# Performance work log

Hardware: AMD Instinct MI355X
Metric: run time of the kernel (lower is better)

The kernel has to match this reference:

```python
import jax, jax.numpy as jnp
import numpy as np

# Dims: B samples, D=2048 backbone feature dim (resnet50 fc.in_features),
B, D, G, R, K, C = 16384, 2048, 8, 6, 3, 16


def setup_inputs() -> dict:
    key = jax.random.key(0)
    k0, k1, k2, k3 = jax.random.split(key, 4)
    feats = jax.random.normal(k0, (B, D), dtype=jnp.float32)          # backbone output (dropout=eval identity)
    roi_ids = jax.random.randint(k1, (B,), 0, G)                       # per-sample routing id (roi_names)
    W_reg = jax.random.normal(k2, (G, R, D), dtype=jnp.float32) * 0.02  # reg_heads[roi].weight
    b_reg = jnp.zeros((G, R), dtype=jnp.float32)                       # reg_heads[roi].bias
    W_cls = jax.random.normal(k3, (G, K, C, D), dtype=jnp.float32) * 0.02  # cls_heads[roi][k].weight
    b_cls = jnp.zeros((G, K, C), dtype=jnp.float32)                    # cls_heads[roi][k].bias
    return {"feats": feats, "roi_ids": roi_ids, "W_reg": W_reg, "b_reg": b_reg,
            "W_cls": W_cls, "b_cls": b_cls}


def reference(feats, roi_ids, W_reg, b_reg, W_cls, b_cls):
    # Original loop applies, per sample i, the Linear heads of roi_names[i].
    # Vectorized: compute all-ROI head outputs densely, then gather the routed one.
    # (Same math per sample; dropout is identity in eval mode.)
    reg_all = jnp.einsum('bd,grd->bgr', feats, W_reg) + b_reg[None]        # [B, G, R]
    cls_all = jnp.einsum('bd,gkcd->bgkc', feats, W_cls) + b_cls[None]      # [B, G, K, C]
    reg = jnp.take_along_axis(reg_all, roi_ids[:, None, None], axis=1)[:, 0]            # [B, R]
    cls = jnp.take_along_axis(cls_all, roi_ids[:, None, None, None], axis=1)[:, 0]      # [B, K, C]
    return reg, cls
```

## Files before the change

kernel.cpp:

```cpp
#include <hip/hip_runtime.h>
#include <hip/hip_bf16.h>

#define NB   16384
#define ND   2048
#define NG   8
#define NR   6
#define NKC  48
#define NOUT 54
#define BM   32
#define KC   128
#define NCH  (ND / KC)
#define CHB  16384
#define LROW 136
#define MAXT (NB / BM + NG)

typedef __attribute__((ext_vector_type(8))) short short8_t;
typedef __attribute__((ext_vector_type(4))) float f32x4;

__device__ __forceinline__ unsigned short f2bf(float x) {
    union { float f; unsigned u; } v; v.f = x;
    unsigned r = v.u + 0x7FFFu + ((v.u >> 16) & 1u);
    return (unsigned short)(r >> 16);
}

__device__ __forceinline__ short8_t cvt8(float4 a, float4 b) {
    short8_t s;
    s[0] = (short)f2bf(a.x); s[1] = (short)f2bf(a.y);
    s[2] = (short)f2bf(a.z); s[3] = (short)f2bf(a.w);
    s[4] = (short)f2bf(b.x); s[5] = (short)f2bf(b.y);
    s[6] = (short)f2bf(b.z); s[7] = (short)f2bf(b.w);
    return s;
}

__device__ __forceinline__ void gl_lds16(const void* g, void* s) {
    __builtin_amdgcn_global_load_lds(
        (const __attribute__((address_space(1))) void*)g,
        (__attribute__((address_space(3))) void*)s,
        16, 0, 0);
}

__global__ void hist_kernel(const int* __restrict__ roi, int* __restrict__ counts) {
    int i = blockIdx.x * 256 + threadIdx.x;
    int g = roi[i];
    int lane = threadIdx.x & 63;
    #pragma unroll
    for (int gg = 0; gg < NG; ++gg) {
        unsigned long long m = __ballot(g == gg);
        if (m && lane == (int)(__ffsll((unsigned long long)m) - 1))
            atomicAdd(&counts[gg], (int)__popcll(m));
    }
}

__global__ void scatter_kernel(const int* __restrict__ roi, const int* __restrict__ counts,
                               int* __restrict__ ranks, int* __restrict__ perm) {
    int off[NG];
    int acc = 0;
    #pragma unroll
    for (int gg = 0; gg < NG; ++gg) { off[gg] = acc; acc += counts[gg]; }
    int i = blockIdx.x * 256 + threadIdx.x;
    int g = roi[i];
    int lane = threadIdx.x & 63;
    #pragma unroll
    for (int gg = 0; gg < NG; ++gg) {
        unsigned long long m = __ballot(g == gg);
        if (!m) continue;
        int leader = (int)(__ffsll((unsigned long long)m) - 1);
        int base = 0;
        if (lane == leader) base = atomicAdd(&ranks[gg], (int)__popcll(m));
        base = __shfl(base, leader);
        if (g == gg) {
            int rank = (int)__popcll(m & ((1ull << lane) - 1ull));
            perm[off[gg] + base + rank] = i;
        }
    }
}

__global__ void scatter1_kernel(const int* __restrict__ roi, int* __restrict__ cnt,
                                int* __restrict__ perm) {
    int i = blockIdx.x * 256 + threadIdx.x;
    int g = roi[i];
    int lane = threadIdx.x & 63;
    #pragma unroll
    for (int gg = 0; gg < NG; ++gg) {
        unsigned long long m = __ballot(g == gg);
        if (!m) continue;
        int leader = (int)(__ffsll((unsigned long long)m) - 1);
        int base = 0;
        if (lane == leader) base = atomicAdd(&cnt[gg], (int)__popcll(m));
        base = __shfl(base, leader);
        if (g == gg) {
            int rank = (int)__popcll(m & ((1ull << lane) - 1ull));
            perm[gg * NB + base + rank] = i;
        }
    }
}

__global__ void wconv_kernel(const float* __restrict__ Wreg, const float* __restrict__ Wcls,
                             short* __restrict__ Wbf) {
    int gi = blockIdx.x * 256 + threadIdx.x;
    int l  = gi & 63;
    int q  = (gi >> 6) & 15;
    int c  = (gi >> 10) & 15;
    int g  = gi >> 14;
    int nh = q >> 3, ks = (q >> 1) & 3, n = q & 1;
    int row = nh * 32 + n * 16 + (l & 15);
    int k   = c * 128 + ks * 32 + (l >> 4) * 8;
    short8_t v = {0, 0, 0, 0, 0, 0, 0, 0};
    if (row < NOUT) {
        const float* s = (row < NR) ? Wreg + (size_t)(g * NR + row) * ND + k
                                    : Wcls + (size_t)(g * NKC + row - NR) * ND + k;
        float4 a = *(const float4*)s;
        float4 b = *(const float4*)(s + 4);
        v = cvt8(a, b);
    }
    *(short8_t*)(Wbf + (size_t)gi * 8) = v;
}

__launch_bounds__(256, 2)
__global__ void gemm_lds_kernel(const float* __restrict__ feats,
                                const short* __restrict__ Wbf,
                                const float* __restrict__ breg, const float* __restrict__ bcls,
                                const int* __restrict__ counts, const int* __restrict__ perm,
                                float* __restrict__ out, int stride) {
    __shared__ __align__(16) char As[2][CHB];
    __shared__ __align__(16) char Bs[2][CHB];
    __shared__ int sRow[BM];

    int ts[NG + 1]; ts[0] = 0;
    int off[NG]; int acc = 0;
    #pragma unroll
    for (int gg = 0; gg < NG; ++gg) {
        int c = counts[gg];
        off[gg] = stride ? gg * stride : acc;
        acc += c;
        ts[gg + 1] = ts[gg] + (c + BM - 1) / BM;
    }
    int b = blockIdx.x;
    if (b >= ts[NG]) return;
    int g = 0;
    #pragma unroll
    for (int gg = 0; gg < NG; ++gg) if (b >= ts[gg + 1]) g = gg + 1;
    int gcnt  = counts[g];
    int goff  = off[g];
    int rbase = (b - ts[g]) * BM;
    int nvalid = gcnt - rbase; if (nvalid > BM) nvalid = BM;

    int tid = threadIdx.x;
    if (tid < BM) {
        int r = rbase + tid;
        if (r >= gcnt) r = gcnt - 1;
        sRow[tid] = perm[goff + r];
    }
    __syncthreads();

    int w = tid >> 6, l = tid & 63, lr = l & 15, lq = l >> 4;
    int mt = w & 1, nh = w >> 1;

    const float* aBase = feats + (size_t)sRow[(w >> 1) * 16 + lr] * ND + lq * 8;
    int ks0 = (w & 1) * 2;
    const short* bBlob = Wbf + (size_t)g * NCH * (CHB / 2) + w * 2048 + l * 8;

    f32x4 acc0 = {0, 0, 0, 0}, acc1 = {0, 0, 0, 0};

#define STAGE(cc, nb) do {                                                    \
        const float* ap_ = aBase + (cc) * KC;                                 \
        gl_lds16(ap_ + (ks0    ) * 32    , &As[nb][(w * 4 + 0) * 1024]);      \
        gl_lds16(ap_ + (ks0    ) * 32 + 4, &As[nb][(w * 4 + 1) * 1024]);      \
        gl_lds16(ap_ + (ks0 + 1) * 32    , &As[nb][(w * 4 + 2) * 1024]);      \
        gl_lds16(ap_ + (ks0 + 1) * 32 + 4, &As[nb][(w * 4 + 3) * 1024]);      \
        const short* bp_ = bBlob + (size_t)(cc) * (CHB / 2);                  \
        gl_lds16(bp_       , &Bs[nb][(w * 4 + 0) * 1024]);                    \
        gl_lds16(bp_ +  512, &Bs[nb][(w * 4 + 1) * 1024]);                    \
        gl_lds16(bp_ + 1024, &Bs[nb][(w * 4 + 2) * 1024]);                    \
        gl_lds16(bp_ + 1536, &Bs[nb][(w * 4 + 3) * 1024]);                    \
    } while (0)

    STAGE(0, 0);
    __syncthreads();

    #pragma unroll 2
    for (int c = 0; c < NCH; ++c) {
        int cb = c & 1;
        if (c + 1 < NCH) STAGE(c + 1, cb ^ 1);
        const float* aRd = (const float*)&As[cb][mt * 8192] + l * 4;
        const short* bRd = (const short*)&Bs[cb][nh * 8192] + l * 8;
        #pragma unroll
        for (int ks = 0; ks < 4; ++ks) {
            float4 a0 = *(const float4*)(aRd + ks * 512);
            float4 a1 = *(const float4*)(aRd + ks * 512 + 256);
            short8_t af = cvt8(a0, a1);
            short8_t b0 = *(const short8_t*)(bRd + ks * 1024);
            short8_t b1 = *(const short8_t*)(bRd + ks * 1024 + 512);
            acc0 = __builtin_amdgcn_mfma_f32_16x16x32_bf16(af, b0, acc0, 0, 0, 0);
            acc1 = __builtin_amdgcn_mfma_f32_16x16x32_bf16(af, b1, acc1, 0, 0, 0);
        }
        __syncthreads();
    }
#undef STAGE

    const int B6 = NB * NR;
    #pragma unroll
    for (int n = 0; n < 2; ++n) {
        f32x4 v = n ? acc1 : acc0;
        int col = nh * 32 + n * 16 + lr;
        if (col < NOUT) {
            #pragma unroll
            for (int j = 0; j < 4; ++j) {
                int row = mt * 16 + lq * 4 + j;
                if (row < nvalid) {
                    int smp = sRow[row];
                    if (col < NR) out[smp * NR + col] = v[j] + breg[g * NR + col];
                    else          out[B6 + smp * NKC + (col - NR)] = v[j] + bcls[g * NKC + (col - NR)];
                }
            }
        }
    }
}

__launch_bounds__(256, 3)
__global__ void gemm_kernel(const float* __restrict__ feats,
                            const float* __restrict__ Wreg, const float* __restrict__ breg,
                            const float* __restrict__ Wcls, const float* __restrict__ bcls,
                            const int* __restrict__ counts, const int* __restrict__ perm,
                            float* __restrict__ out, int stride) {
    __shared__ __align__(16) short Bsh[2][64][LROW];
    __shared__ int sRow[BM];

    int ts[NG + 1]; ts[0] = 0;
    int off[NG]; int acc = 0;
    #pragma unroll
    for (int gg = 0; gg < NG; ++gg) {
        int c = counts[gg];
        off[gg] = stride ? gg * stride : acc;
        acc += c;
        ts[gg + 1] = ts[gg] + (c + BM - 1) / BM;
    }
    int b = blockIdx.x;
    if (b >= ts[NG]) return;
    int g = 0;
    #pragma unroll
    for (int gg = 0; gg < NG; ++gg) if (b >= ts[gg + 1]) g = gg + 1;
    int gcnt  = counts[g];
    int goff  = off[g];
    int rbase = (b - ts[g]) * BM;
    int nvalid = gcnt - rbase; if (nvalid > BM) nvalid = BM;

    int tid = threadIdx.x;
    if (tid < BM) {
        int r = rbase + tid;
        if (r >= gcnt) r = gcnt - 1;
        sRow[tid] = perm[goff + r];
    }
    __syncthreads();

    int rB = tid >> 2;
    int cq = tid & 3;
    const float* wsrc = nullptr;
    if (rB < NR)        wsrc = Wreg + ((size_t)g * NR + rB) * ND + cq * 32;
    else if (rB < NOUT) wsrc = Wcls + ((size_t)g * NKC + (rB - NR)) * ND + cq * 32;

    int w = tid >> 6, l = tid & 63, lr = l & 15, lq = l >> 4;
    int mt = w & 1, nh = w >> 1;
    const float* aptr = feats + (size_t)sRow[mt * 16 + lr] * ND + lq * 8;
    const short* brp = (const short*)&Bsh[0][0][0] + (nh * 32 + lr) * LROW + lq * 8;

    f32x4 acc0 = {0, 0, 0, 0}, acc1 = {0, 0, 0, 0};
    float4 rb[8];

    if (wsrc) {
        #pragma unroll
        for (int i = 0; i < 8; ++i) rb[i] = *(const float4*)(wsrc + 4 * i);
    } else {
        #pragma unroll
        for (int i = 0; i < 8; ++i) rb[i] = make_float4(0.f, 0.f, 0.f, 0.f);
    }
    {
        short* bw = &Bsh[0][rB][cq * 32];
        #pragma unroll
        for (int j = 0; j < 4; ++j) *(short8_t*)(bw + 8 * j) = cvt8(rb[2 * j], rb[2 * j + 1]);
    }
    __syncthreads();

    #pragma unroll
    for (int c = 0; c < NCH; ++c) {
        const int cur = c & 1, nxt = cur ^ 1;
        if (c + 1 < NCH && wsrc) {
            const float* s = wsrc + (c + 1) * KC;
            #pragma unroll
            for (int i = 0; i < 8; ++i) rb[i] = *(const float4*)(s + 4 * i);
        }
        const short* bp = brp + cur * (64 * LROW);
        const float* ap = aptr + c * KC;
        #pragma unroll
        for (int ks = 0; ks < 4; ++ks) {
            float4 a0 = *(const float4*)(ap + ks * 32);
            float4 a1 = *(const float4*)(ap + ks * 32 + 4);
            short8_t af = cvt8(a0, a1);
            short8_t b0 = *(const short8_t*)(bp + ks * 32);
            short8_t b1 = *(const short8_t*)(bp + 16 * LROW + ks * 32);
            acc0 = __builtin_amdgcn_mfma_f32_16x16x32_bf16(af, b0, acc0, 0, 0, 0);
            acc1 = __builtin_amdgcn_mfma_f32_16x16x32_bf16(af, b1, acc1, 0, 0, 0);
        }
        if (c + 1 < NCH && wsrc) {
            short* bw = &Bsh[nxt][rB][cq * 32];
            #pragma unroll
            for (int j = 0; j < 4; ++j) *(short8_t*)(bw + 8 * j) = cvt8(rb[2 * j], rb[2 * j + 1]);
        } else if (c + 1 < NCH) {
            short8_t z = {0,0,0,0,0,0,0,0};
            short* bw = &Bsh[nxt][rB][cq * 32];
            #pragma unroll
            for (int j = 0; j < 4; ++j) *(short8_t*)(bw + 8 * j) = z;
        }
        __syncthreads();
    }

    const int B6 = NB * NR;
    #pragma unroll
    for (int n = 0; n < 2; ++n) {
        f32x4 v = n ? acc1 : acc0;
        int col = nh * 32 + n * 16 + lr;
        if (col < NOUT) {
            #pragma unroll
            for (int j = 0; j < 4; ++j) {
                int row = mt * 16 + lq * 4 + j;
                if (row < nvalid) {
                    int smp = sRow[row];
                    if (col < NR) out[smp * NR + col] = v[j] + breg[g * NR + col];
                    else          out[B6 + smp * NKC + (col - NR)] = v[j] + bcls[g * NKC + (col - NR)];
                }
            }
        }
    }
}

__global__ void fallback_kernel(const float* __restrict__ feats, const int* __restrict__ roi,
                                const float* __restrict__ Wreg, const float* __restrict__ breg,
                                const float* __restrict__ Wcls, const float* __restrict__ bcls,
                                float* __restrict__ out) {
    int i = blockIdx.x;
    int lane = threadIdx.x;
    int g = roi[i];
    const float* frow = feats + (size_t)i * ND;
    float f[32];
    #pragma unroll
    for (int q = 0; q < 32; ++q) f[q] = frow[lane + 64 * q];
    for (int o = 0; o < NOUT; ++o) {
        const float* wrow = (o < NR) ? Wreg + ((size_t)g * NR + o) * ND
                                     : Wcls + ((size_t)g * NKC + (o - NR)) * ND;
        float p = 0.f;
        #pragma unroll
        for (int q = 0; q < 32; ++q) p += f[q] * wrow[lane + 64 * q];
        #pragma unroll
        for (int s = 32; s; s >>= 1) p += __shfl_xor(p, s);
        if (lane == 0) {
            if (o < NR) out[i * NR + o] = p + breg[g * NR + o];
            else        out[NB * NR + i * NKC + (o - NR)] = p + bcls[g * NKC + (o - NR)];
        }
    }
}

extern "C" void kernel_launch(void* const* d_in, const int* in_sizes, int n_in,
                              void* d_out, int out_size, void* d_ws, size_t ws_size,
                              hipStream_t stream) {
    const float* feats = (const float*)d_in[0];
    const int*   roi   = (const int*)d_in[1];
    const float* Wreg  = (const float*)d_in[2];
    const float* breg  = (const float*)d_in[3];
    const float* Wcls  = (const float*)d_in[4];
    const float* bcls  = (const float*)d_in[5];
    float* out = (float*)d_out;

    const size_t wbfBytes = (size_t)NG * NCH * CHB;
    const size_t need_t1 = wbfBytes + 256 + (size_t)NG * NB * 4;
    const size_t need_t2 = wbfBytes + 256 + (size_t)NB * 4;
    const size_t need_t3 = 256 + (size_t)NB * 4;

    if (ws_size >= need_t1) {
        short* Wbf = (short*)d_ws;
        int* cnt  = (int*)((char*)d_ws + wbfBytes);
        int* perm = cnt + 64;
        hipMemsetAsync(cnt, 0, 8 * sizeof(int), stream);
        wconv_kernel<<<512, 256, 0, stream>>>(Wreg, Wcls, Wbf);
        scatter1_kernel<<<NB / 256, 256, 0, stream>>>(roi, cnt, perm);
        gemm_lds_kernel<<<MAXT, 256, 0, stream>>>(feats, Wbf, breg, bcls, cnt, perm, out, NB);
    } else if (ws_size >= need_t2) {
        short* Wbf = (short*)d_ws;
        int* counts = (int*)((char*)d_ws + wbfBytes);
        int* ranks  = counts + 8;
        int* perm   = counts + 64;
        hipMemsetAsync(counts, 0, 16 * sizeof(int), stream);
        wconv_kernel<<<512, 256, 0, stream>>>(Wreg, Wcls, Wbf);
        hist_kernel<<<NB / 256, 256, 0, stream>>>(roi, counts);
        scatter_kernel<<<NB / 256, 256, 0, stream>>>(roi, counts, ranks, perm);
        gemm_lds_kernel<<<MAXT, 256, 0, stream>>>(feats, Wbf, breg, bcls, counts, perm, out, 0);
    } else if (ws_size >= need_t3) {
        int* counts = (int*)d_ws;
        int* ranks  = counts + 8;
        int* perm   = counts + 64;
        hipMemsetAsync(counts, 0, 16 * sizeof(int), stream);
        hist_kernel<<<NB / 256, 256, 0, stream>>>(roi, counts);
        scatter_kernel<<<NB / 256, 256, 0, stream>>>(roi, counts, ranks, perm);
        gemm_kernel<<<MAXT, 256, 0, stream>>>(feats, Wreg, breg, Wcls, bcls, counts, perm, out, 0);
    } else {
        fallback_kernel<<<NB, 64, 0, stream>>>(feats, roi, Wreg, breg, Wcls, bcls, out);
    }
}
```

Before: 84.83 us.

## Use triple-buffered LDS pipeline with smaller K chunks and explicit vmcnt waits

Replaces the double-buffered GEMM, which used 128-wide K chunks and a full __syncthreads per chunk, with a three-slot LDS ring that uses 64-wide chunks and prefetches two chunks ahead. Explicit s_waitcnt vmcnt counts and raw barriers let loads stay in flight across iterations instead of draining them all. The bf16 weight blob layout is changed to match the new chunking. The medium-workspace path is dropped, which leaves a gap in fallback coverage, and the extra barrier per chunk adds sync overhead.

```diff
diff --git a/kernel.cpp b/kernel.cpp
--- a/kernel.cpp
+++ b/kernel.cpp
@@ -8,10 +8,12 @@
 #define NKC  48
 #define NOUT 54
 #define BM   32
+#define KC3  64
+#define NCH3 (ND / KC3)
+#define SLOT 16384
+#define LROW 136
 #define KC   128
 #define NCH  (ND / KC)
-#define CHB  16384
-#define LROW 136
 #define MAXT (NB / BM + NG)
 
 typedef __attribute__((ext_vector_type(8))) short short8_t;
@@ -38,6 +40,11 @@
         (__attribute__((address_space(3))) void*)s,
         16, 0, 0);
 }
+
+#define WAITV(N) do { asm volatile("s_waitcnt vmcnt(" #N ")" ::: "memory"); \
+                      __builtin_amdgcn_sched_barrier(0); } while (0)
+#define BARRIER() do { __builtin_amdgcn_s_barrier(); \
+                       __builtin_amdgcn_sched_barrier(0); } while (0)
 
 __global__ void hist_kernel(const int* __restrict__ roi, int* __restrict__ counts) {
     int i = blockIdx.x * 256 + threadIdx.x;
@@ -97,14 +104,15 @@
 
 __global__ void wconv_kernel(const float* __restrict__ Wreg, const float* __restrict__ Wcls,
                              short* __restrict__ Wbf) {
-    int gi = blockIdx.x * 256 + threadIdx.x;
-    int l  = gi & 63;
-    int q  = (gi >> 6) & 15;
-    int c  = (gi >> 10) & 15;
-    int g  = gi >> 14;
-    int nh = q >> 3, ks = (q >> 1) & 3, n = q & 1;
+    int u = blockIdx.x * 256 + threadIdx.x;
+    int l  = u & 63;
+    int ks = (u >> 6) & 1;
+    int n  = (u >> 7) & 1;
+    int nh = (u >> 8) & 1;
+    int c  = (u >> 9) & 31;
+    int g  = u >> 14;
     int row = nh * 32 + n * 16 + (l & 15);
-    int k   = c * 128 + ks * 32 + (l >> 4) * 8;
+    int k   = c * 64 + ks * 32 + (l >> 4) * 8;
     short8_t v = {0, 0, 0, 0, 0, 0, 0, 0};
     if (row < NOUT) {
         const float* s = (row < NR) ? Wreg + (size_t)(g * NR + row) * ND + k
@@ -113,26 +121,25 @@
         float4 b = *(const float4*)(s + 4);
         v = cvt8(a, b);
     }
-    *(short8_t*)(Wbf + (size_t)gi * 8) = v;
+    *(short8_t*)(Wbf + (size_t)u * 8) = v;
 }
 
 __launch_bounds__(256, 2)
-__global__ void gemm_lds_kernel(const float* __restrict__ feats,
-                                const short* __restrict__ Wbf,
-                                const float* __restrict__ breg, const float* __restrict__ bcls,
-                                const int* __restrict__ counts, const int* __restrict__ perm,
-                                float* __restrict__ out, int stride) {
-    __shared__ __align__(16) char As[2][CHB];
-    __shared__ __align__(16) char Bs[2][CHB];
+__global__ void gemm_p3_kernel(const float* __restrict__ feats,
+                               const short* __restrict__ Wbf,
+                               const float* __restrict__ breg, const float* __restrict__ bcls,
+                               const int* __restrict__ counts, const int* __restrict__ perm,
+                               float* __restrict__ out, int stride) {
+    __shared__ __align__(16) char lds[3][SLOT];
     __shared__ int sRow[BM];
 
     int ts[NG + 1]; ts[0] = 0;
-    int off[NG]; int acc = 0;
+    int off[NG]; int acc_ = 0;
     #pragma unroll
     for (int gg = 0; gg < NG; ++gg) {
         int c = counts[gg];
-        off[gg] = stride ? gg * stride : acc;
-        acc += c;
+        off[gg] = stride ? gg * stride : acc_;
+        acc_ += c;
         ts[gg + 1] = ts[gg] + (c + BM - 1) / BM;
     }
     int b = blockIdx.x;
@@ -156,45 +163,47 @@
     int w = tid >> 6, l = tid & 63, lr = l & 15, lq = l >> 4;
     int mt = w & 1, nh = w >> 1;
 
-    const float* aBase = feats + (size_t)sRow[(w >> 1) * 16 + lr] * ND + lq * 8;
-    int ks0 = (w & 1) * 2;
-    const short* bBlob = Wbf + (size_t)g * NCH * (CHB / 2) + w * 2048 + l * 8;
+    const float* paBase = feats + (size_t)sRow[mt * 16 + lr] * ND + nh * 32 + lq * 8;
+    char* ldsA = &lds[0][0] + (mt * 4096 + nh * 2048);
+    const short* pbBase = Wbf + ((size_t)g * 32 * 8 + (nh * 2 + mt) * 2) * 512 + l * 8;
+    char* ldsB = &lds[0][8192] + (nh * 4096 + mt * 2048);
+
+#define STAGE(cc, sl) do {                                                     \
+        const float* a_ = paBase + (size_t)(cc) * KC3;                         \
+        gl_lds16(a_,     ldsA + (sl) * SLOT);                                  \
+        gl_lds16(a_ + 4, ldsA + (sl) * SLOT + 1024);                           \
+        const short* b_ = pbBase + (size_t)(cc) * 4096;                        \
+        gl_lds16(b_,       ldsB + (sl) * SLOT);                                \
+        gl_lds16(b_ + 512, ldsB + (sl) * SLOT + 1024);                         \
+    } while (0)
 
     f32x4 acc0 = {0, 0, 0, 0}, acc1 = {0, 0, 0, 0};
 
-#define STAGE(cc, nb) do {                                                    \
-        const float* ap_ = aBase + (cc) * KC;                                 \
-        gl_lds16(ap_ + (ks0    ) * 32    , &As[nb][(w * 4 + 0) * 1024]);      \
-        gl_lds16(ap_ + (ks0    ) * 32 + 4, &As[nb][(w * 4 + 1) * 1024]);      \
-        gl_lds16(ap_ + (ks0 + 1) * 32    , &As[nb][(w * 4 + 2) * 1024]);      \
-        gl_lds16(ap_ + (ks0 + 1) * 32 + 4, &As[nb][(w * 4 + 3) * 1024]);      \
-        const short* bp_ = bBlob + (size_t)(cc) * (CHB / 2);                  \
-        gl_lds16(bp_       , &Bs[nb][(w * 4 + 0) * 1024]);                    \
-        gl_lds16(bp_ +  512, &Bs[nb][(w * 4 + 1) * 1024]);                    \
-        gl_lds16(bp_ + 1024, &Bs[nb][(w * 4 + 2) * 1024]);                    \
-        gl_lds16(bp_ + 1536, &Bs[nb][(w * 4 + 3) * 1024]);                    \
-    } while (0)
-
-    STAGE(0, 0);
-    __syncthreads();
-
-    #pragma unroll 2
-    for (int c = 0; c < NCH; ++c) {
-        int cb = c & 1;
-        if (c + 1 < NCH) STAGE(c + 1, cb ^ 1);
-        const float* aRd = (const float*)&As[cb][mt * 8192] + l * 4;
-        const short* bRd = (const short*)&Bs[cb][nh * 8192] + l * 8;
-        #pragma unroll
-        for (int ks = 0; ks < 4; ++ks) {
-            float4 a0 = *(const float4*)(aRd + ks * 512);
-            float4 a1 = *(const float4*)(aRd + ks * 512 + 256);
-            short8_t af = cvt8(a0, a1);
-            short8_t b0 = *(const short8_t*)(bRd + ks * 1024);
-            short8_t b1 = *(const short8_t*)(bRd + ks * 1024 + 512);
-            acc0 = __builtin_amdgcn_mfma_f32_16x16x32_bf16(af, b0, acc0, 0, 0, 0);
-            acc1 = __builtin_amdgcn_mfma_f32_16x16x32_bf16(af, b1, acc1, 0, 0, 0);
-        }
-        __syncthreads();
+    STAGE(0, 0); STAGE(1, 1);
+
+    #pragma unroll
+    for (int c = 0; c < NCH3; ++c) {
+        const int sl = c % 3;
+        if (c + 2 < NCH3) STAGE(c + 2, (c + 2) % 3);
+        if (c < NCH3 - 2)       WAITV(8);
+        else if (c == NCH3 - 2) WAITV(4);
+        else                    WAITV(0);
+        BARRIER();
+        {
+            const char* sa = &lds[sl][mt * 4096];
+            const char* sb = &lds[sl][8192 + nh * 4096];
+            #pragma unroll
+            for (int ks = 0; ks < 2; ++ks) {
+                float4 a0 = *(const float4*)(sa + ks * 2048 + l * 16);
+                float4 a1 = *(const float4*)(sa + ks * 2048 + 1024 + l * 16);
+                short8_t af = cvt8(a0, a1);
+                short8_t b0 = *(const short8_t*)(sb + ks * 1024 + l * 16);
+                short8_t b1 = *(const short8_t*)(sb + 2048 + ks * 1024 + l * 16);
+                acc0 = __builtin_amdgcn_mfma_f32_16x16x32_bf16(af, b0, acc0, 0, 0, 0);
+                acc1 = __builtin_amdgcn_mfma_f32_16x16x32_bf16(af, b1, acc1, 0, 0, 0);
+            }
+        }
+        BARRIER();
     }
 #undef STAGE
 
@@ -370,9 +379,8 @@
     const float* bcls  = (const float*)d_in[5];
     float* out = (float*)d_out;
 
-    const size_t wbfBytes = (size_t)NG * NCH * CHB;
+    const size_t wbfBytes = (size_t)NG * 131072 * 2;
     const size_t need_t1 = wbfBytes + 256 + (size_t)NG * NB * 4;
-    const size_t need_t2 = wbfBytes + 256 + (size_t)NB * 4;
     const size_t need_t3 = 256 + (size_t)NB * 4;
 
     if (ws_size >= need_t1) {
@@ -382,17 +390,7 @@
         hipMemsetAsync(cnt, 0, 8 * sizeof(int), stream);
         wconv_kernel<<<512, 256, 0, stream>>>(Wreg, Wcls, Wbf);
         scatter1_kernel<<<NB / 256, 256, 0, stream>>>(roi, cnt, perm);
-        gemm_lds_kernel<<<MAXT, 256, 0, stream>>>(feats, Wbf, breg, bcls, cnt, perm, out, NB);
-    } else if (ws_size >= need_t2) {
-        short* Wbf = (short*)d_ws;
-        int* counts = (int*)((char*)d_ws + wbfBytes);
-        int* ranks  = counts + 8;
-        int* perm   = counts + 64;
-        hipMemsetAsync(counts, 0, 16 * sizeof(int), stream);
-        wconv_kernel<<<512, 256, 0, stream>>>(Wreg, Wcls, Wbf);
-        hist_kernel<<<NB / 256, 256, 0, stream>>>(roi, counts);
-        scatter_kernel<<<NB / 256, 256, 0, stream>>>(roi, counts, ranks, perm);
-        gemm_lds_kernel<<<MAXT, 256, 0, stream>>>(feats, Wbf, breg, bcls, counts, perm, out, 0);
+        gemm_p3_kernel<<<MAXT, 256, 0, stream>>>(feats, Wbf, breg, bcls, cnt, perm, out, NB);
     } else if (ws_size >= need_t3) {
         int* counts = (int*)d_ws;
         int* ranks  = counts + 8;
```

Result: faster. 69.91 us (-17.6%).
